# Kernel tuning notes

Hardware: AMD Instinct MI355X
Metric: run time of the kernel (lower is better)

The kernel has to match this reference:

```python
import jax, jax.numpy as jnp
import numpy as np

N_IN, N_OUT, D_IN, D_HID, STYLE = 16384, 16384, 64, 256, 64
E = 1048576
EPS_BN = 1e-5
EPS_ADA = 1e-8
SLOPE = 0.2

def leaky(x):
    return jnp.where(x >= 0, x, SLOPE * x)

def bn_train(h, g, b):
    # BatchNorm1d, training mode: batch stats over dim 0, biased variance
    m = jnp.mean(h, axis=0)
    v = jnp.var(h, axis=0)
    return (h - m) * jax.lax.rsqrt(v + EPS_BN) * g + b

def adain(h, style, w1, b1, w2, b2):
    # per-node instance norm over feature axis (unbiased std, as torch.std),
    # style-conditioned per-feature gamma/beta
    mean = jnp.mean(h, axis=1, keepdims=True)
    std = jnp.std(h, axis=1, ddof=1, keepdims=True)
    gamma = w1 @ style + b1
    beta = w2 @ style + b2
    return gamma * (h - mean) / (std + EPS_ADA) + beta

def gat_conv(h, src, dst, W, att_src, att_dst, bias):
    # PyG GATConv, heads=1: linear -> edge attention -> segment softmax -> scatter
    xs = h @ W.T                          # [N, D_IN]
    a_s = xs @ att_src                    # [N]
    a_d = xs @ att_dst                    # [N]
    e = leaky(a_s[src] + a_d[dst])        # [E]
    emax = jax.ops.segment_max(e, dst, num_segments=N_OUT)
    emax = jnp.where(jnp.isfinite(emax), emax, 0.0)
    ex = jnp.exp(e - emax[dst])
    den = jax.ops.segment_sum(ex, dst, num_segments=N_OUT)
    alpha = ex / den[dst]                 # softmax over incoming edges per dst
    out = jax.ops.segment_sum(alpha[:, None] * xs[src], dst, num_segments=N_OUT)
    return out + bias

def setup_inputs():
    key = jax.random.key(0)
    ks = jax.random.split(key, 24)
    p = lambda k, shape: jax.random.normal(k, shape, jnp.float32) * 0.05
    return {
        "x": jax.random.normal(ks[0], (N_IN, D_IN), jnp.float32),
        "style": jax.random.normal(ks[1], (STYLE,), jnp.float32),
        "edge_index": jax.random.randint(ks[2], (2, E), 0, N_OUT, jnp.int32),
        "trs_w": p(ks[3], (N_OUT, N_IN)), "trs_b": jnp.zeros((N_OUT,), jnp.float32),
        "bn2_g": jnp.ones((N_OUT,), jnp.float32), "bn2_b": jnp.zeros((N_OUT,), jnp.float32),
        "fc1_w": p(ks[4], (D_HID, D_IN)), "fc1_b": jnp.zeros((D_HID,), jnp.float32),
        "bn1_g": jnp.ones((D_HID,), jnp.float32), "bn1_b": jnp.zeros((D_HID,), jnp.float32),
        "gat_w": p(ks[5], (D_IN, D_HID)),
        "gat_att_src": p(ks[6], (D_IN,)), "gat_att_dst": p(ks[7], (D_IN,)),
        "gat_b": jnp.zeros((D_IN,), jnp.float32),
        "a1_w1": p(ks[8], (D_IN, STYLE)), "a1_b1": jnp.zeros((D_IN,), jnp.float32),
        "a1_w2": p(ks[9], (D_IN, STYLE)), "a1_b2": jnp.zeros((D_IN,), jnp.float32),
        "a2_w1": p(ks[10], (D_HID, STYLE)), "a2_b1": jnp.zeros((D_HID,), jnp.float32),
        "a2_w2": p(ks[11], (D_HID, STYLE)), "a2_b2": jnp.zeros((D_HID,), jnp.float32),
        "a3_w1": p(ks[12], (D_IN, STYLE)), "a3_b1": jnp.zeros((D_IN,), jnp.float32),
        "a3_w2": p(ks[13], (D_IN, STYLE)), "a3_b2": jnp.zeros((D_IN,), jnp.float32),
    }

def reference(x, style, edge_index, trs_w, trs_b, bn2_g, bn2_b, fc1_w, fc1_b, bn1_g, bn1_b, gat_w, gat_att_src, gat_att_dst, gat_b, a1_w1, a1_b1, a1_w2, a1_b2, a2_w1, a2_b1, a2_w2, a2_b2, a3_w1, a3_b1, a3_w2, a3_b2):
    h = x.T @ trs_w.T + trs_b                 # [D_IN, N_OUT]
    h = leaky(bn_train(h, bn2_g, bn2_b))      # dropout: eval-mode identity
    h = h.T                                    # [N_OUT, D_IN]
    h = adain(h, style, a1_w1, a1_b1, a1_w2, a1_b2)
    h = leaky(bn_train(h @ fc1_w.T + fc1_b, bn1_g, bn1_b))  # [N_OUT, D_HID]
    h = adain(h, style, a2_w1, a2_b1, a2_w2, a2_b2)
    src, dst = edge_index[0], edge_index[1]
    h = leaky(gat_conv(h, src, dst, gat_w, gat_att_src, gat_att_dst, gat_b))
    h = adain(h, style, a3_w1, a3_b1, a3_w2, a3_b2)
    return h
```

## Files before the change

### kernel.cpp

```cpp
#include <hip/hip_runtime.h>
#include <hip/hip_bf16.h>

#define N_NODES 16384
#define NEDGE   1048576

typedef __attribute__((ext_vector_type(4))) float f32x4;
typedef __attribute__((ext_vector_type(4))) unsigned u32x4;
typedef __attribute__((ext_vector_type(8))) short bf16x8;
typedef __attribute__((ext_vector_type(8))) unsigned short u16x8;
typedef unsigned short u16;

__device__ __forceinline__ short f2bf(float f) {
  union { float f; unsigned u; } v; v.f = f;
  unsigned r = v.u + 0x7FFFu + ((v.u >> 16) & 1u);
  return (short)(r >> 16);
}
__device__ __forceinline__ float bf2f(unsigned short h) {
  union { unsigned u; float f; } v; v.u = ((unsigned)h) << 16;
  return v.f;
}
__device__ __forceinline__ unsigned pk2(float lo, float hi) {
  __hip_bfloat162 h = __float22bfloat162_rn(make_float2(lo, hi));
  return *reinterpret_cast<unsigned*>(&h);
}
__device__ __forceinline__ bf16x8 cvt8(f32x4 a, f32x4 b) {
  u32x4 u;
  u[0] = pk2(a[0], a[1]); u[1] = pk2(a[2], a[3]);
  u[2] = pk2(b[0], b[1]); u[3] = pk2(b[2], b[3]);
  return __builtin_bit_cast(bf16x8, u);
}
__device__ __forceinline__ float red16(float v) {
  v += __shfl_xor(v, 1); v += __shfl_xor(v, 2);
  v += __shfl_xor(v, 4); v += __shfl_xor(v, 8);
  return v;
}
__device__ __forceinline__ float red64(float v) {
  v += __shfl_xor(v, 1); v += __shfl_xor(v, 2); v += __shfl_xor(v, 4);
  v += __shfl_xor(v, 8); v += __shfl_xor(v, 16); v += __shfl_xor(v, 32);
  return v;
}
__device__ __forceinline__ float lrelu(float x){ return x >= 0.f ? x : 0.2f*x; }

__global__ __launch_bounds__(256) void k_prep(
    const float* __restrict__ x, const float* __restrict__ style,
    const float* __restrict__ fc1_w, const float* __restrict__ gat_w,
    const float* __restrict__ a1w1, const float* __restrict__ a1b1,
    const float* __restrict__ a1w2, const float* __restrict__ a1b2,
    const float* __restrict__ a2w1, const float* __restrict__ a2b1,
    const float* __restrict__ a2w2, const float* __restrict__ a2b2,
    const float* __restrict__ a3w1, const float* __restrict__ a3b1,
    const float* __restrict__ a3w2, const float* __restrict__ a3b2,
    u16* __restrict__ xpk, u16* __restrict__ fc1pk, u16* __restrict__ gatpk,
    float* __restrict__ gb, const int* __restrict__ dst, int* __restrict__ cnt)
{
  if (blockIdx.x >= 531) {
    int t = ((blockIdx.x - 531) << 8) + threadIdx.x;
    #pragma unroll
    for (int i = 0; i < 4; ++i) atomicAdd(&cnt[dst[t + i*262144]], 1);
    return;
  }
  int tid = blockIdx.x * 256 + threadIdx.x;
  if (tid < 131072) {
    int lane = tid & 63;
    int kt = tid >> 8, nt = (tid >> 6) & 3;
    int k0 = kt*32 + (lane>>4)*8, c = nt*16 + (lane&15);
    bf16x8 o;
    #pragma unroll
    for (int j = 0; j < 8; ++j) o[j] = f2bf(x[(size_t)(k0+j)*64 + c]);
    ((bf16x8*)xpk)[tid] = o;
  } else if (tid < 133120) {
    int t2 = tid - 131072;
    int lane = t2 & 63, kt = t2 >> 10, nt = (t2 >> 6) & 15;
    int k0 = kt*32 + (lane>>4)*8, c = nt*16 + (lane&15);
    bf16x8 o;
    #pragma unroll
    for (int j = 0; j < 8; ++j) o[j] = f2bf(fc1_w[(size_t)c*64 + k0 + j]);
    ((bf16x8*)fc1pk)[t2] = o;
  } else if (tid < 135168) {
    int t3 = tid - 133120;
    int lane = t3 & 63, kt = t3 >> 8, nt = (t3 >> 6) & 3;
    int k0 = kt*32 + (lane>>4)*8, c = nt*16 + (lane&15);
    bf16x8 o;
    #pragma unroll
    for (int j = 0; j < 8; ++j) o[j] = f2bf(gat_w[(size_t)c*256 + k0 + j]);
    ((bf16x8*)gatpk)[t3] = o;
  } else if (tid < 135936) {
    int t4 = tid - 135168;
    const float* wp; const float* bp; float* op; int d;
    if (t4 < 64)       { wp=a1w1; bp=a1b1; op=gb;       d=t4; }
    else if (t4 < 128) { wp=a1w2; bp=a1b2; op=gb+64;    d=t4-64; }
    else if (t4 < 384) { wp=a2w1; bp=a2b1; op=gb+128;   d=t4-128; }
    else if (t4 < 640) { wp=a2w2; bp=a2b2; op=gb+384;   d=t4-384; }
    else if (t4 < 704) { wp=a3w1; bp=a3b1; op=gb+640;   d=t4-640; }
    else               { wp=a3w2; bp=a3b2; op=gb+704;   d=t4-704; }
    float s = bp[d];
    for (int k = 0; k < 64; ++k) s += wp[(size_t)d*64 + k] * style[k];
    op[d] = s;
  }
}

__global__ __launch_bounds__(256, 4) void k_gemm12(
    const float* __restrict__ W, const u16* __restrict__ xpk,
    const float* __restrict__ trs_b, const float* __restrict__ bn2_g,
    const float* __restrict__ bn2_b, const float* __restrict__ g1,
    const float* __restrict__ be1,
    const u16* __restrict__ fc1pk, const float* __restrict__ fc1_b,
    float* __restrict__ H3, float* __restrict__ colsum, float* __restrict__ colsq,
    const int* __restrict__ cnt, int* __restrict__ off, int* __restrict__ cur)
{
  if (blockIdx.x == 1024) {
    __shared__ int ps[256];
    int t = threadIdx.x;
    int base = t * 64;
    int s = 0;
    for (int i = 0; i < 64; ++i) s += cnt[base + i];
    ps[t] = s;
    __syncthreads();
    for (int d = 1; d < 256; d <<= 1) {
      int v = (t >= d) ? ps[t - d] : 0;
      __syncthreads();
      ps[t] += v;
      __syncthreads();
    }
    int run = ps[t] - s;
    for (int i = 0; i < 64; ++i) {
      off[base + i] = run; cur[base + i] = run;
      run += cnt[base + i];
    }
    return;
  }
  const int tid  = threadIdx.x;
  const int lane = tid & 63;
  const int wv   = tid >> 6;
  const int jb   = blockIdx.x << 4;
  const int c0   = lane & 15, kg = lane >> 4;
  const int sw   = c0 & 7;

  __shared__ __align__(16) float lbuf[2][4096];
  __shared__ float h2t[16 * 68];

  const float* gsrc[4];
  int ldst[4];
  #pragma unroll
  for (int i = 0; i < 4; ++i) {
    int r = wv + (i << 2);
    gsrc[i] = W + (size_t)(jb + r) * 16384 + (size_t)((lane ^ (r & 7)) << 2);
    ldst[i] = ((r << 6) + lane) << 2;
  }

  const int it0 = blockIdx.x & 63;
  f32x4 z = {0.f,0.f,0.f,0.f};
  f32x4 acc = z;
  f32x4 P[4], Q[4];

  {
    int kk0 = it0 << 8;
    #pragma unroll
    for (int i = 0; i < 4; ++i) {
      f32x4 v = __builtin_nontemporal_load((const f32x4*)(gsrc[i] + kk0));
      *(f32x4*)&lbuf[0][ldst[i]] = v;
    }
    int kk1 = ((it0 + 1) & 63) << 8;
    #pragma unroll
    for (int i = 0; i < 4; ++i)
      P[i] = __builtin_nontemporal_load((const f32x4*)(gsrc[i] + kk1));
    int kk2 = ((it0 + 2) & 63) << 8;
    #pragma unroll
    for (int i = 0; i < 4; ++i)
      Q[i] = __builtin_nontemporal_load((const f32x4*)(gsrc[i] + kk2));
  }
  __syncthreads();

  const bf16x8* xb = ((const bf16x8*)xpk) + (wv << 6) + lane;

#define G1_BODY(ITX, R) do {                                                 \
    const int it_ = (ITX);                                                   \
    {                                                                        \
      float* lo_ = lbuf[(it_ + 1) & 1];                                      \
      _Pragma("unroll")                                                      \
      for (int i = 0; i < 4; ++i) *(f32x4*)&lo_[ldst[i]] = R[i];             \
    }                                                                        \
    if (it_ <= 60) {                                                         \
      int kk_ = ((it_ + 3 + it0) & 63) << 8;                                 \
      _Pragma("unroll")                                                      \
      for (int i = 0; i < 4; ++i)                                            \
        R[i] = __builtin_nontemporal_load((const f32x4*)(gsrc[i] + kk_));    \
    }                                                                        \
    {                                                                        \
      int ktg0_ = ((it_ + it0) & 63) << 3;                                   \
      const float* lb_ = lbuf[it_ & 1] + (c0 << 8);                          \
      const bf16x8* bp_ = xb + (size_t)ktg0_ * 256;                          \
      _Pragma("unroll")                                                      \
      for (int kt = 0; kt < 8; ++kt) {                                       \
        int u0_ = (kt << 3) + (kg << 1);                                     \
        f32x4 a0 = *(const f32x4*)(lb_ + ((u0_ ^ sw) << 2));                 \
        f32x4 a1 = *(const f32x4*)(lb_ + (((u0_ + 1) ^ sw) << 2));           \
        bf16x8 b = bp_[(size_t)kt << 8];                                     \
        acc = __builtin_amdgcn_mfma_f32_16x16x32_bf16(cvt8(a0, a1), b, acc, 0,0,0); \
      }                                                                      \
    }                                                                        \
    __syncthreads();                                                         \
  } while (0)

  for (int i2 = 0; i2 < 31; ++i2) {
    G1_BODY(2 * i2,     P);
    G1_BODY(2 * i2 + 1, Q);
  }
  G1_BODY(62, P);
  {
    int ktg0 = ((63 + it0) & 63) << 3;
    const float* lb = lbuf[1] + (c0 << 8);
    const bf16x8* bp = xb + (size_t)ktg0 * 256;
    #pragma unroll
    for (int kt = 0; kt < 8; ++kt) {
      int u0 = (kt << 3) + (kg << 1);
      f32x4 a0 = *(const f32x4*)(lb + ((u0 ^ sw) << 2));
      f32x4 a1 = *(const f32x4*)(lb + (((u0 + 1) ^ sw) << 2));
      bf16x8 b = bp[(size_t)kt << 8];
      acc = __builtin_amdgcn_mfma_f32_16x16x32_bf16(cvt8(a0, a1), b, acc, 0,0,0);
    }
  }
#undef G1_BODY
  __syncthreads();

  #pragma unroll
  for (int i = 0; i < 4; ++i)
    h2t[((kg << 2) + i) * 68 + (wv << 4) + c0] = acc[i];
  __syncthreads();

  #pragma unroll
  for (int i = 0; i < 4; ++i) {
    int jr = (wv << 2) + i;
    int j  = jb + jr;
    float v = h2t[jr * 68 + lane] + trs_b[j];
    float s = red64(v), q = red64(v * v);
    float mean = s * 0.015625f;
    float var  = q * 0.015625f - mean * mean;
    float inv  = rsqrtf(var + 1e-5f) * bn2_g[j];
    v = lrelu((v - mean) * inv + bn2_b[j]);
    s = red64(v); q = red64(v * v);
    mean = s * 0.015625f;
    var  = q * 0.015625f - mean * mean;
    float sd = sqrtf(fmaxf(var, 0.f) * (64.f / 63.f));
    float id = 1.f / (sd + 1e-8f);
    h2t[jr * 68 + lane] = g1[lane] * (v - mean) * id + be1[lane];
  }
  __syncthreads();

  const float* ha = h2t + c0 * 68 + (kg << 3);
  bf16x8 a0 = cvt8(*(const f32x4*)ha,        *(const f32x4*)(ha+4));
  bf16x8 a1 = cvt8(*(const f32x4*)(ha+32),   *(const f32x4*)(ha+36));
  const bf16x8* fpv = ((const bf16x8*)fc1pk) + lane;
  f32x4 acc2[4] = {z,z,z,z};
  #pragma unroll
  for (int q = 0; q < 4; ++q) {
    int nt = (wv << 2) | q;
    acc2[q] = __builtin_amdgcn_mfma_f32_16x16x32_bf16(a0, fpv[nt*64],      acc2[q], 0,0,0);
    acc2[q] = __builtin_amdgcn_mfma_f32_16x16x32_bf16(a1, fpv[(16+nt)*64], acc2[q], 0,0,0);
  }
  #pragma unroll
  for (int q = 0; q < 4; ++q) {
    int c = (((wv << 2) | q) << 4) + c0;
    float bias = fc1_b[c];
    float cs = 0.f, cq = 0.f;
    #pragma unroll
    for (int r = 0; r < 4; ++r) {
      float v = acc2[q][r] + bias;
      H3[(size_t)(jb + (kg<<2) + r) * 256 + c] = v;
      cs += v; cq += v*v;
    }
    cs += __shfl_xor(cs, 16); cs += __shfl_xor(cs, 32);
    cq += __shfl_xor(cq, 16); cq += __shfl_xor(cq, 32);
    if (kg == 0) { atomicAdd(&colsum[c], cs); atomicAdd(&colsq[c], cq); }
  }
}

__global__ __launch_bounds__(256) void k_gemm3(
    const float* __restrict__ H3, const float* __restrict__ colsum,
    const float* __restrict__ colsq, const float* __restrict__ bn1_g,
    const float* __restrict__ bn1_b, const float* __restrict__ gb,
    const u16* __restrict__ gatpk,
    const float* __restrict__ att_s, const float* __restrict__ att_d,
    u16* __restrict__ xs, float* __restrict__ a_s, float* __restrict__ a_d,
    const int* __restrict__ src, const int* __restrict__ dstE,
    int* __restrict__ cur, int* __restrict__ ssrc)
{
  if (blockIdx.x >= 1024) {
    int t = ((blockIdx.x - 1024) << 8) + threadIdx.x;
    #pragma unroll
    for (int i = 0; i < 4; ++i) {
      int e = t + i * 262144;
      int s = src[e], d = dstE[e];
      int p = atomicAdd(&cur[d], 1);
      ssrc[p] = s;
    }
    return;
  }
  const int lane = threadIdx.x & 63, wv = threadIdx.x >> 6;
  const int jb = blockIdx.x << 4;
  const int c0 = lane & 15, kg = lane >> 4;
  const int row = jb + c0;
  const int col0 = (wv << 6) + (kg << 3);
  const float* g2  = gb + 128;
  const float* be2 = gb + 384;

  f32x4 w4[4];
  float ps = 0.f, pq = 0.f;
  #pragma unroll
  for (int kk = 0; kk < 2; ++kk) {
    #pragma unroll
    for (int h = 0; h < 2; ++h) {
      int c = col0 + kk*32 + h*4;
      f32x4 v  = *(const f32x4*)(H3 + (size_t)row*256 + c);
      f32x4 cm = *(const f32x4*)(colsum + c);
      f32x4 cq = *(const f32x4*)(colsq + c);
      f32x4 gg = *(const f32x4*)(bn1_g + c);
      f32x4 bb = *(const f32x4*)(bn1_b + c);
      f32x4 t;
      #pragma unroll
      for (int i = 0; i < 4; ++i) {
        float m  = cm[i] * (1.f/16384.f);
        float va = cq[i] * (1.f/16384.f) - m*m;
        float u  = (v[i]-m) * rsqrtf(va + 1e-5f) * gg[i] + bb[i];
        u = lrelu(u);
        t[i] = u; ps += u; pq += u*u;
      }
      w4[kk*2+h] = t;
    }
  }
  ps += __shfl_xor(ps, 16); ps += __shfl_xor(ps, 32);
  pq += __shfl_xor(pq, 16); pq += __shfl_xor(pq, 32);
  __shared__ float sps[64], sqs[64];
  if (kg == 0) { sps[(wv<<4) + c0] = ps; sqs[(wv<<4) + c0] = pq; }
  __syncthreads();
  float rs = sps[c0] + sps[16+c0] + sps[32+c0] + sps[48+c0];
  float rq = sqs[c0] + sqs[16+c0] + sqs[32+c0] + sqs[48+c0];
  float mean = rs * (1.f/256.f);
  float var  = rq * (1.f/256.f) - mean*mean;
  float sd   = sqrtf(fmaxf(var, 0.f) * (256.f/255.f));
  float id   = 1.f / (sd + 1e-8f);
  bf16x8 afr[2];
  #pragma unroll
  for (int kk = 0; kk < 2; ++kk) {
    f32x4 o[2];
    #pragma unroll
    for (int h = 0; h < 2; ++h) {
      int c = col0 + kk*32 + h*4;
      f32x4 ga = *(const f32x4*)(g2 + c);
      f32x4 bd = *(const f32x4*)(be2 + c);
      #pragma unroll
      for (int i = 0; i < 4; ++i) o[h][i] = ga[i]*(w4[kk*2+h][i]-mean)*id + bd[i];
    }
    afr[kk] = cvt8(o[0], o[1]);
  }
  const bf16x8* bpv = ((const bf16x8*)gatpk) + lane;
  f32x4 z = {0.f,0.f,0.f,0.f};
  f32x4 acc[4] = {z,z,z,z};
  #pragma unroll
  for (int kk = 0; kk < 2; ++kk) {
    int kt = (wv << 1) | kk;
    #pragma unroll
    for (int nt = 0; nt < 4; ++nt)
      acc[nt] = __builtin_amdgcn_mfma_f32_16x16x32_bf16(afr[kk], bpv[((kt<<2)+nt)*64], acc[nt], 0,0,0);
  }
  __shared__ float lred[3 * 16 * 64];
  if (wv) {
    float* rp = lred + ((wv - 1) << 10) + lane;
    #pragma unroll
    for (int nt = 0; nt < 4; ++nt)
      #pragma unroll
      for (int r = 0; r < 4; ++r) rp[((nt<<2)+r)<<6] = acc[nt][r];
  }
  __syncthreads();
  if (wv) return;
  float as0 = att_s[c0], as1 = att_s[c0+16], as2 = att_s[c0+32], as3 = att_s[c0+48];
  float ad0 = att_d[c0], ad1 = att_d[c0+16], ad2 = att_d[c0+32], ad3 = att_d[c0+48];
  const float* rp = lred + lane;
  #pragma unroll
  for (int r = 0; r < 4; ++r) {
    int j = jb + (kg << 2) + r;
    float v[4];
    #pragma unroll
    for (int nt = 0; nt < 4; ++nt) {
      int idx = ((nt<<2)+r)<<6;
      v[nt] = acc[nt][r] + rp[idx] + rp[idx+1024] + rp[idx+2048];
    }
    u16* op = xs + (size_t)j * 64 + c0;
    op[0]  = (u16)f2bf(v[0]);
    op[16] = (u16)f2bf(v[1]);
    op[32] = (u16)f2bf(v[2]);
    op[48] = (u16)f2bf(v[3]);
    float ss = red16(v[0]*as0 + v[1]*as1 + v[2]*as2 + v[3]*as3);
    float dd = red16(v[0]*ad0 + v[1]*ad1 + v[2]*ad2 + v[3]*ad3);
    if (c0 == 0) { a_s[j] = ss; a_d[j] = dd; }
  }
}

__global__ __launch_bounds__(256) void k_gat(
    const int* __restrict__ cnt, const int* __restrict__ off,
    const int* __restrict__ ssrc, const float* __restrict__ a_s,
    const float* __restrict__ a_d,
    const u16* __restrict__ xs, const float* __restrict__ gat_b,
    const float* __restrict__ g3, const float* __restrict__ be3,
    float* __restrict__ out)
{
  const int lane = threadIdx.x & 63, wv = threadIdx.x >> 6;
  const int j = (blockIdx.x << 2) | wv;
  const int n = cnt[j], beg = off[j];
  const int c8 = (lane & 7) << 3;
  const int eq = lane >> 3;
  const float adj = a_d[j];
  float acc[8] = {0.f,0.f,0.f,0.f,0.f,0.f,0.f,0.f};
  float den = 0.f;
  if (n > 0) {
    for (int ch = 0; ch < n; ch += 64) {
      int k = ch + lane;
      bool ok = k < n;
      int   s = ok ? ssrc[beg + k] : 0;
      float p = ok ? __expf(lrelu(a_s[s] + adj)) : 0.f;
      den += p;
      int m = n - ch; if (m > 64) m = 64;
      int iters = (m + 7) >> 3;
      for (int i = 0; i < iters; ++i) {
        int idx = (i << 3) | eq;
        float pi = __shfl(p, idx);
        int   si = __shfl(s, idx);
        u16x8 hv = *(const u16x8*)(xs + (size_t)si * 64 + c8);
        #pragma unroll
        for (int t = 0; t < 8; ++t) acc[t] += pi * bf2f(hv[t]);
      }
    }
    den = red64(den);
    #pragma unroll
    for (int t = 0; t < 8; ++t) {
      acc[t] += __shfl_xor(acc[t], 8);
      acc[t] += __shfl_xor(acc[t], 16);
      acc[t] += __shfl_xor(acc[t], 32);
    }
    float rd = 1.f / den;
    #pragma unroll
    for (int t = 0; t < 8; ++t) acc[t] *= rd;
  }
  float vv[8];
  float s8 = 0.f, q8 = 0.f;
  #pragma unroll
  for (int t = 0; t < 8; ++t) {
    float v = lrelu(acc[t] + gat_b[c8 + t]);
    vv[t] = v; s8 += v; q8 += v * v;
  }
  s8 += __shfl_xor(s8, 1); s8 += __shfl_xor(s8, 2); s8 += __shfl_xor(s8, 4);
  q8 += __shfl_xor(q8, 1); q8 += __shfl_xor(q8, 2); q8 += __shfl_xor(q8, 4);
  float mean = s8 * (1.f/64.f);
  float var  = q8 * (1.f/64.f) - mean*mean;
  float sd   = sqrtf(fmaxf(var, 0.f) * (64.f/63.f));
  float id   = 1.f / (sd + 1e-8f);
  if (eq == 0) {
    f32x4 o0, o1;
    #pragma unroll
    for (int t = 0; t < 4; ++t) {
      o0[t] = g3[c8+t]   * (vv[t]  -mean)*id + be3[c8+t];
      o1[t] = g3[c8+4+t] * (vv[4+t]-mean)*id + be3[c8+4+t];
    }
    float* op = out + (size_t)j * 64 + c8;
    *(f32x4*)op       = o0;
    *(f32x4*)(op + 4) = o1;
  }
}

extern "C" void kernel_launch(void* const* d_in, const int* in_sizes, int n_in,
                              void* d_out, int out_size, void* d_ws, size_t ws_size,
                              hipStream_t stream) {
  (void)in_sizes; (void)n_in; (void)out_size; (void)ws_size;
  const float* x      = (const float*)d_in[0];
  const float* style  = (const float*)d_in[1];
  const int*   ei     = (const int*)d_in[2];
  const float* trs_w  = (const float*)d_in[3];
  const float* trs_b  = (const float*)d_in[4];
  const float* bn2_g  = (const float*)d_in[5];
  const float* bn2_b  = (const float*)d_in[6];
  const float* fc1_w  = (const float*)d_in[7];
  const float* fc1_b  = (const float*)d_in[8];
  const float* bn1_g  = (const float*)d_in[9];
  const float* bn1_b  = (const float*)d_in[10];
  const float* gat_w  = (const float*)d_in[11];
  const float* att_s  = (const float*)d_in[12];
  const float* att_d  = (const float*)d_in[13];
  const float* gat_b  = (const float*)d_in[14];
  const float* a1w1   = (const float*)d_in[15];
  const float* a1b1   = (const float*)d_in[16];
  const float* a1w2   = (const float*)d_in[17];
  const float* a1b2   = (const float*)d_in[18];
  const float* a2w1   = (const float*)d_in[19];
  const float* a2b1   = (const float*)d_in[20];
  const float* a2w2   = (const float*)d_in[21];
  const float* a2b2   = (const float*)d_in[22];
  const float* a3w1   = (const float*)d_in[23];
  const float* a3b1   = (const float*)d_in[24];
  const float* a3w2   = (const float*)d_in[25];
  const float* a3b2   = (const float*)d_in[26];

  char* ws = (char*)d_ws;
  u16*   xpk    = (u16*)(ws);
  u16*   fc1pk  = (u16*)(ws + 2097152);
  u16*   gatpk  = (u16*)(ws + 2129920);
  float* gb     = (float*)(ws + 2162688);
  float* H3     = (float*)(ws + 6361088);
  u16*   xs     = (u16*)(ws + 39915520);
  float* as_    = (float*)(ws + 44109824);
  float* ad_    = (float*)(ws + 44175360);
  float* colsum = (float*)(ws + 44240896);
  float* colsq  = (float*)(ws + 44241920);
  int*   cnt    = (int*)(ws + 44242944);
  int*   off    = (int*)(ws + 44308480);
  int*   cur    = (int*)(ws + 44374016);
  int*   ssrc   = (int*)(ws + 44439552);

  hipMemsetAsync(colsum, 0, 2048, stream);
  hipMemsetAsync(cnt, 0, 65536, stream);

  k_prep<<<1555, 256, 0, stream>>>(x, style, fc1_w, gat_w,
      a1w1, a1b1, a1w2, a1b2, a2w1, a2b1, a2w2, a2b2, a3w1, a3b1, a3w2, a3b2,
      xpk, fc1pk, gatpk, gb, ei + NEDGE, cnt);
  k_gemm12<<<1025, 256, 0, stream>>>(trs_w, xpk, trs_b, bn2_g, bn2_b,
      gb, gb + 64, fc1pk, fc1_b, H3, colsum, colsq, cnt, off, cur);
  k_gemm3<<<2048, 256, 0, stream>>>(H3, colsum, colsq, bn1_g, bn1_b, gb,
      gatpk, att_s, att_d, xs, as_, ad_, ei, ei + NEDGE, cur, ssrc);
  k_gat<<<4096, 256, 0, stream>>>(cnt, off, ssrc, as_, ad_, xs, gat_b,
      gb + 640, gb + 704, (float*)d_out);
}
```

Baseline: 375.9 us.

## Split K across waves in projection GEMM and reduce partials through LDS

Each wave now takes a quarter of every K chunk across all four output column tiles, instead of all of K for one column tile. This cuts each wave's LDS reads and fp32-to-bf16 conversions of the streamed weight tile by a factor of four. The four partial accumulators are then summed through the reused lbuf space, and wave 0 alone runs the BatchNorm/AdaIN epilogue using 16-lane reductions. The cost is an extra LDS reduction step and a serialized epilogue on a single wave.

New measurement: 372.1 us. No clear change (-1.0%).

```diff
diff --git a/kernel.cpp b/kernel.cpp
--- a/kernel.cpp
+++ b/kernel.cpp
@@ -137,7 +137,6 @@
   const int sw   = c0 & 7;
 
   __shared__ __align__(16) float lbuf[2][4096];
-  __shared__ float h2t[16 * 68];
 
   const float* gsrc[4];
   int ldst[4];
@@ -150,7 +149,7 @@
 
   const int it0 = blockIdx.x & 63;
   f32x4 z = {0.f,0.f,0.f,0.f};
-  f32x4 acc = z;
+  f32x4 acc[4] = {z,z,z,z};
   f32x4 P[4], Q[4];
 
   {
@@ -171,7 +170,25 @@
   }
   __syncthreads();
 
-  const bf16x8* xb = ((const bf16x8*)xpk) + (wv << 6) + lane;
+  const bf16x8* xpb = ((const bf16x8*)xpk) + lane;
+
+#define G1_COMPUTE(ITX) do {                                                 \
+    int ktg0_ = ((ITX) + it0 & 63) << 3;                                     \
+    const float* lb_ = lbuf[(ITX) & 1] + (c0 << 8);                          \
+    _Pragma("unroll")                                                        \
+    for (int kk = 0; kk < 2; ++kk) {                                         \
+      int ktl_ = (wv << 1) | kk;                                             \
+      int u0_ = (ktl_ << 3) + (kg << 1);                                     \
+      f32x4 a0 = *(const f32x4*)(lb_ + ((u0_ ^ sw) << 2));                   \
+      f32x4 a1 = *(const f32x4*)(lb_ + (((u0_ + 1) ^ sw) << 2));             \
+      bf16x8 a = cvt8(a0, a1);                                               \
+      const bf16x8* bp_ = xpb + (size_t)((ktg0_ + ktl_) << 2) * 64;          \
+      acc[0] = __builtin_amdgcn_mfma_f32_16x16x32_bf16(a, bp_[0],   acc[0], 0,0,0); \
+      acc[1] = __builtin_amdgcn_mfma_f32_16x16x32_bf16(a, bp_[64],  acc[1], 0,0,0); \
+      acc[2] = __builtin_amdgcn_mfma_f32_16x16x32_bf16(a, bp_[128], acc[2], 0,0,0); \
+      acc[3] = __builtin_amdgcn_mfma_f32_16x16x32_bf16(a, bp_[192], acc[3], 0,0,0); \
+    }                                                                        \
+  } while (0)
 
 #define G1_BODY(ITX, R) do {                                                 \
     const int it_ = (ITX);                                                   \
@@ -186,19 +203,7 @@
       for (int i = 0; i < 4; ++i)                                            \
         R[i] = __builtin_nontemporal_load((const f32x4*)(gsrc[i] + kk_));    \
     }                                                                        \
-    {                                                                        \
-      int ktg0_ = ((it_ + it0) & 63) << 3;                                   \
-      const float* lb_ = lbuf[it_ & 1] + (c0 << 8);                          \
-      const bf16x8* bp_ = xb + (size_t)ktg0_ * 256;                          \
-      _Pragma("unroll")                                                      \
-      for (int kt = 0; kt < 8; ++kt) {                                       \
-        int u0_ = (kt << 3) + (kg << 1);                                     \
-        f32x4 a0 = *(const f32x4*)(lb_ + ((u0_ ^ sw) << 2));                 \
-        f32x4 a1 = *(const f32x4*)(lb_ + (((u0_ + 1) ^ sw) << 2));           \
-        bf16x8 b = bp_[(size_t)kt << 8];                                     \
-        acc = __builtin_amdgcn_mfma_f32_16x16x32_bf16(cvt8(a0, a1), b, acc, 0,0,0); \
-      }                                                                      \
-    }                                                                        \
+    G1_COMPUTE(it_);                                                         \
     __syncthreads();                                                         \
   } while (0)
 
@@ -207,43 +212,57 @@
     G1_BODY(2 * i2 + 1, Q);
   }
   G1_BODY(62, P);
-  {
-    int ktg0 = ((63 + it0) & 63) << 3;
-    const float* lb = lbuf[1] + (c0 << 8);
-    const bf16x8* bp = xb + (size_t)ktg0 * 256;
-    #pragma unroll
-    for (int kt = 0; kt < 8; ++kt) {
-      int u0 = (kt << 3) + (kg << 1);
-      f32x4 a0 = *(const f32x4*)(lb + ((u0 ^ sw) << 2));
-      f32x4 a1 = *(const f32x4*)(lb + (((u0 + 1) ^ sw) << 2));
-      bf16x8 b = bp[(size_t)kt << 8];
-      acc = __builtin_amdgcn_mfma_f32_16x16x32_bf16(cvt8(a0, a1), b, acc, 0,0,0);
-    }
-  }
+  G1_COMPUTE(63);
 #undef G1_BODY
+#undef G1_COMPUTE
   __syncthreads();
 
-  #pragma unroll
-  for (int i = 0; i < 4; ++i)
-    h2t[((kg << 2) + i) * 68 + (wv << 4) + c0] = acc[i];
+  float* lred = &lbuf[0][0];
+  float* h2t  = &lbuf[1][0];
+  if (wv) {
+    float* rp = lred + ((wv - 1) << 10) + lane;
+    #pragma unroll
+    for (int nt = 0; nt < 4; ++nt)
+      #pragma unroll
+      for (int r = 0; r < 4; ++r) rp[((nt<<2)+r)<<6] = acc[nt][r];
+  }
   __syncthreads();
-
-  #pragma unroll
-  for (int i = 0; i < 4; ++i) {
-    int jr = (wv << 2) + i;
-    int j  = jb + jr;
-    float v = h2t[jr * 68 + lane] + trs_b[j];
-    float s = red64(v), q = red64(v * v);
-    float mean = s * 0.015625f;
-    float var  = q * 0.015625f - mean * mean;
-    float inv  = rsqrtf(var + 1e-5f) * bn2_g[j];
-    v = lrelu((v - mean) * inv + bn2_b[j]);
-    s = red64(v); q = red64(v * v);
-    mean = s * 0.015625f;
-    var  = q * 0.015625f - mean * mean;
-    float sd = sqrtf(fmaxf(var, 0.f) * (64.f / 63.f));
-    float id = 1.f / (sd + 1e-8f);
-    h2t[jr * 68 + lane] = g1[lane] * (v - mean) * id + be1[lane];
+  if (wv == 0) {
+    float val[4][4];
+    const float* rp = lred + lane;
+    #pragma unroll
+    for (int nt = 0; nt < 4; ++nt)
+      #pragma unroll
+      for (int r = 0; r < 4; ++r) {
+        int idx = ((nt<<2)+r)<<6;
+        val[nt][r] = acc[nt][r] + rp[idx] + rp[idx+1024] + rp[idx+2048];
+      }
+    #pragma unroll
+    for (int r = 0; r < 4; ++r) {
+      int jr = (kg << 2) + r;
+      int j  = jb + jr;
+      float tb = trs_b[j];
+      float v0 = val[0][r]+tb, v1 = val[1][r]+tb, v2 = val[2][r]+tb, v3 = val[3][r]+tb;
+      float s = red16(v0+v1+v2+v3);
+      float q = red16(v0*v0+v1*v1+v2*v2+v3*v3);
+      float mean = s * 0.015625f;
+      float var  = q * 0.015625f - mean*mean;
+      float inv  = rsqrtf(var + 1e-5f) * bn2_g[j];
+      float bb   = bn2_b[j];
+      v0 = lrelu((v0-mean)*inv + bb); v1 = lrelu((v1-mean)*inv + bb);
+      v2 = lrelu((v2-mean)*inv + bb); v3 = lrelu((v3-mean)*inv + bb);
+      s = red16(v0+v1+v2+v3);
+      q = red16(v0*v0+v1*v1+v2*v2+v3*v3);
+      mean = s * 0.015625f;
+      var  = q * 0.015625f - mean*mean;
+      float sd = sqrtf(fmaxf(var, 0.f) * (64.f/63.f));
+      float id = 1.f / (sd + 1e-8f);
+      float* hr = h2t + jr * 68;
+      hr[c0]    = g1[c0]    * (v0-mean)*id + be1[c0];
+      hr[c0+16] = g1[c0+16] * (v1-mean)*id + be1[c0+16];
+      hr[c0+32] = g1[c0+32] * (v2-mean)*id + be1[c0+32];
+      hr[c0+48] = g1[c0+48] * (v3-mean)*id + be1[c0+48];
+    }
   }
   __syncthreads();
 
```
